# Optimization experiments

Measured on AMD Instinct MI355X. Metric: run time of the kernel, lower is better.

The kernel has to match this reference:

```python
import jax, jax.numpy as jnp
import numpy as np

DT = 1.0 / 200.0  # imu_freq = 200
EPS = 1e-8

def _skew(v):  # [B,3] -> [B,3,3]
    x, y, z = v[:, 0], v[:, 1], v[:, 2]
    zero = jnp.zeros_like(x)
    return jnp.stack([zero, -z, y, z, zero, -x, -y, x, zero], axis=-1).reshape(-1, 3, 3)

def _axis_angle_to_R(w, dt):
    # Rodrigues: R = I + sin(th) K + (1-cos(th)) K^2, th = ||w||*dt
    n = jnp.linalg.norm(w, axis=-1, keepdims=True)          # [B,1]
    theta = n[:, 0] * dt                                     # [B]
    axis = w / (n + EPS)
    K = _skew(axis)
    I = jnp.eye(3, dtype=w.dtype)
    s = jnp.sin(theta)[:, None, None]
    c = jnp.cos(theta)[:, None, None]
    return I + s * K + (1.0 - c) * jnp.einsum('bij,bjk->bik', K, K)

def _R_to_axis_angle(R):
    tr = jnp.trace(R, axis1=-2, axis2=-1)
    angle = jnp.arccos(jnp.clip((tr - 1.0) / 2.0, -1.0 + 1e-7, 1.0 - 1e-7))
    axis = jnp.stack([R[:, 2, 1] - R[:, 1, 2],
                      R[:, 0, 2] - R[:, 2, 0],
                      R[:, 1, 0] - R[:, 0, 1]], axis=-1)
    axis = axis / (2.0 * jnp.sin(angle)[:, None] + EPS)
    return axis, angle

def _aa_to_quat(axis, angle):  # (w, x, y, z)
    h = angle / 2.0
    return jnp.concatenate([jnp.cos(h)[:, None], axis * jnp.sin(h)[:, None]], axis=-1)

def setup_inputs() -> dict:
    key = jax.random.key(0)
    input_seq = jax.random.normal(key, (512, 4096, 6), dtype=jnp.float32)
    return {"input_seq": input_seq}

def reference(input_seq):
    B, T, _ = input_seq.shape
    dtype = input_seq.dtype
    w = jnp.transpose(input_seq[:, :, :3], (1, 0, 2))  # [T,B,3] gyro
    a = jnp.transpose(input_seq[:, :, 3:], (1, 0, 2))  # [T,B,3] accel
    dt = jnp.asarray(DT, dtype)
    dt2_half = dt * dt / 2.0

    dR0 = jnp.broadcast_to(jnp.eye(3, dtype=dtype), (B, 3, 3))
    dv0 = jnp.zeros((B, 3), dtype)
    dp0 = jnp.zeros((B, 3), dtype)

    def step(carry, inp):
        dR, dv, dp = carry
        w_k, a_k = inp
        dR = jnp.einsum('bij,bjk->bik', dR, _axis_angle_to_R(w_k, dt))
        Ra = jnp.einsum('bij,bj->bi', dR, a_k)
        dv = dv + Ra * dt
        dp = dp + dv * dt + Ra * dt2_half  # uses already-updated dv, as in torch code
        axis, angle = _R_to_axis_angle(dR)
        q = _aa_to_quat(axis, angle)
        return (dR, dv, dp), (dp, dv, q)

    _, (ps, vs, qs) = jax.lax.scan(step, (dR0, dv0, dp0), (w, a))
    ps = jnp.transpose(ps, (1, 0, 2))  # [B,T,3]
    vs = jnp.transpose(vs, (1, 0, 2))  # [B,T,3]
    qs = jnp.transpose(qs, (1, 0, 2))  # [B,T,4]
    return jnp.concatenate([input_seq, ps, qs, vs], axis=2)  # [B,T,16]
```

## Files before the change

### kernel.cpp

```cpp
#include <hip/hip_runtime.h>
#include <math.h>

#define T_LEN 4096
#define CHUNK 8
#define NTHR  512
#define ESTRIDE 15

__device__ __forceinline__ void make_A(float wx, float wy, float wz, float* A) {
    const float dt = 1.0f / 200.0f;
    float n = sqrtf(wx*wx + wy*wy + wz*wz);
    float theta = n * dt;
    float inv = 1.0f / (n + 1e-8f);
    float x = wx * inv, y = wy * inv, z = wz * inv;
    float s = sinf(theta);
    float c = cosf(theta);
    float oc = 1.0f - c;
    A[0] = 1.0f + oc * (-(y*y + z*z));
    A[1] = -s*z + oc * (x*y);
    A[2] =  s*y + oc * (x*z);
    A[3] =  s*z + oc * (x*y);
    A[4] = 1.0f + oc * (-(x*x + z*z));
    A[5] = -s*x + oc * (y*z);
    A[6] = -s*y + oc * (x*z);
    A[7] =  s*x + oc * (y*z);
    A[8] = 1.0f + oc * (-(x*x + y*y));
}

__device__ __forceinline__ void matmul3(const float* R, const float* A, float* N) {
#pragma unroll
    for (int i = 0; i < 3; ++i) {
        N[i*3+0] = R[i*3+0]*A[0] + R[i*3+1]*A[3] + R[i*3+2]*A[6];
        N[i*3+1] = R[i*3+0]*A[1] + R[i*3+1]*A[4] + R[i*3+2]*A[7];
        N[i*3+2] = R[i*3+0]*A[2] + R[i*3+1]*A[5] + R[i*3+2]*A[8];
    }
}

__device__ __forceinline__ void step(float* R, float* v, float* p,
                                     float wx, float wy, float wz,
                                     float ax, float ay, float az) {
    const float dt   = 1.0f / 200.0f;
    const float dt2h = dt * dt * 0.5f;
    float A[9], N[9];
    make_A(wx, wy, wz, A);
    matmul3(R, A, N);
#pragma unroll
    for (int i = 0; i < 9; ++i) R[i] = N[i];
    float rax = R[0]*ax + R[1]*ay + R[2]*az;
    float ray = R[3]*ax + R[4]*ay + R[5]*az;
    float raz = R[6]*ax + R[7]*ay + R[8]*az;
    v[0] += rax*dt; v[1] += ray*dt; v[2] += raz*dt;
    p[0] += v[0]*dt + rax*dt2h;
    p[1] += v[1]*dt + ray*dt2h;
    p[2] += v[2]*dt + raz*dt2h;
}

__global__ __launch_bounds__(NTHR)
void preint_kernel(const float* __restrict__ in, float* __restrict__ out) {
    const int b = blockIdx.x;
    const int t = threadIdx.x;
    const float dt = 1.0f / 200.0f;

    const float* bin  = in  + (size_t)b * T_LEN * 6;
    float*       bout = out + (size_t)b * T_LEN * 16;

    float in_reg[CHUNK * 6];
    {
        const float4* src4 = (const float4*)(bin + (size_t)t * CHUNK * 6);
#pragma unroll
        for (int i = 0; i < (CHUNK * 6) / 4; ++i) {
            float4 u = src4[i];
            in_reg[i*4+0] = u.x; in_reg[i*4+1] = u.y;
            in_reg[i*4+2] = u.z; in_reg[i*4+3] = u.w;
        }
    }

    float R[9] = {1,0,0, 0,1,0, 0,0,1};
    float v[3] = {0,0,0};
    float p[3] = {0,0,0};
#pragma unroll
    for (int k = 0; k < CHUNK; ++k) {
        const float* u = in_reg + k * 6;
        step(R, v, p, u[0], u[1], u[2], u[3], u[4], u[5]);
    }

    __shared__ float lds[NTHR * ESTRIDE];
    float* e = lds + t * ESTRIDE;
#pragma unroll
    for (int i = 0; i < 9; ++i) e[i] = R[i];
    e[9]  = v[0]; e[10] = v[1]; e[11] = v[2];
    e[12] = p[0]; e[13] = p[1]; e[14] = p[2];
    __syncthreads();

    for (int d = 1; d < NTHR; d <<= 1) {
        float L[15];
        const bool act = (t >= d);
        if (act) {
            const float* src = lds + (t - d) * ESTRIDE;
#pragma unroll
            for (int i = 0; i < 15; ++i) L[i] = src[i];
        }
        __syncthreads();
        if (act) {
            const float tau2 = (float)(d * CHUNK) * dt;
            float NA[9];
            matmul3(L, R, NA);
            float nb0 = L[9]  + L[0]*v[0] + L[1]*v[1] + L[2]*v[2];
            float nb1 = L[10] + L[3]*v[0] + L[4]*v[1] + L[5]*v[2];
            float nb2 = L[11] + L[6]*v[0] + L[7]*v[1] + L[8]*v[2];
            float nc0 = L[12] + tau2*L[9]  + L[0]*p[0] + L[1]*p[1] + L[2]*p[2];
            float nc1 = L[13] + tau2*L[10] + L[3]*p[0] + L[4]*p[1] + L[5]*p[2];
            float nc2 = L[14] + tau2*L[11] + L[6]*p[0] + L[7]*p[1] + L[8]*p[2];
#pragma unroll
            for (int i = 0; i < 9; ++i) R[i] = NA[i];
            v[0] = nb0; v[1] = nb1; v[2] = nb2;
            p[0] = nc0; p[1] = nc1; p[2] = nc2;
#pragma unroll
            for (int i = 0; i < 9; ++i) e[i] = R[i];
            e[9]  = v[0]; e[10] = v[1]; e[11] = v[2];
            e[12] = p[0]; e[13] = p[1]; e[14] = p[2];
        }
        __syncthreads();
    }

    float S[9]  = {1,0,0, 0,1,0, 0,0,1};
    float sv[3] = {0,0,0};
    float sp[3] = {0,0,0};
    if (t > 0) {
        const float* src = lds + (t - 1) * ESTRIDE;
#pragma unroll
        for (int i = 0; i < 9; ++i) S[i] = src[i];
        sv[0] = src[9];  sv[1] = src[10]; sv[2] = src[11];
        sp[0] = src[12]; sp[1] = src[13]; sp[2] = src[14];
    }

#pragma unroll
    for (int kk = 0; kk < CHUNK; kk += 2) {
        float4 row[8];
#pragma unroll
        for (int j = 0; j < 2; ++j) {
            const int k = kk + j;
            const float* u = in_reg + k * 6;
            step(S, sv, sp, u[0], u[1], u[2], u[3], u[4], u[5]);

            float tr  = S[0] + S[4] + S[8];
            float ca  = fminf(fmaxf(0.5f * (tr - 1.0f), -1.0f + 1e-7f), 1.0f - 1e-7f);
            float qw  = sqrtf(0.5f * (1.0f + ca));
            float i4  = 0.25f / qw;
            float qx  = (S[7] - S[5]) * i4;
            float qy  = (S[2] - S[6]) * i4;
            float qz  = (S[3] - S[1]) * i4;

            row[j*4+0] = make_float4(u[0], u[1], u[2], u[3]);
            row[j*4+1] = make_float4(u[4], u[5], sp[0], sp[1]);
            row[j*4+2] = make_float4(sp[2], qw, qx, qy);
            row[j*4+3] = make_float4(qz, sv[0], sv[1], sv[2]);
        }
        float4* orow = (float4*)(bout + (size_t)(t * CHUNK + kk) * 16);
#pragma unroll
        for (int i = 0; i < 8; ++i) orow[i] = row[i];
    }
}

extern "C" void kernel_launch(void* const* d_in, const int* in_sizes, int n_in,
                              void* d_out, int out_size, void* d_ws, size_t ws_size,
                              hipStream_t stream) {
    const float* in = (const float*)d_in[0];
    float* out = (float*)d_out;
    const int B = in_sizes[0] / (T_LEN * 6);
    preint_kernel<<<dim3(B), dim3(NTHR), 0, stream>>>(in, out);
}
```

Measured before the change: 206.6 us.

## Replace LDS block scan with wave-shuffle scan plus cross-wave totals

```diff
diff --git a/kernel.cpp b/kernel.cpp
--- a/kernel.cpp
+++ b/kernel.cpp
@@ -4,26 +4,26 @@
 #define T_LEN 4096
 #define CHUNK 8
 #define NTHR  512
-#define ESTRIDE 15
+#define NWAVE (NTHR / 64)
 
 __device__ __forceinline__ void make_A(float wx, float wy, float wz, float* A) {
-    const float dt = 1.0f / 200.0f;
-    float n = sqrtf(wx*wx + wy*wy + wz*wz);
-    float theta = n * dt;
-    float inv = 1.0f / (n + 1e-8f);
-    float x = wx * inv, y = wy * inv, z = wz * inv;
-    float s = sinf(theta);
-    float c = cosf(theta);
-    float oc = 1.0f - c;
-    A[0] = 1.0f + oc * (-(y*y + z*z));
-    A[1] = -s*z + oc * (x*y);
-    A[2] =  s*y + oc * (x*z);
-    A[3] =  s*z + oc * (x*y);
-    A[4] = 1.0f + oc * (-(x*x + z*z));
-    A[5] = -s*x + oc * (y*z);
-    A[6] = -s*y + oc * (x*z);
-    A[7] =  s*x + oc * (y*z);
-    A[8] = 1.0f + oc * (-(x*x + y*y));
+    const float dt  = 1.0f / 200.0f;
+    const float dt2 = dt * dt;
+    float n2 = wx*wx + wy*wy + wz*wz;
+    float t2 = n2 * dt2;
+    float s_ = dt  * (1.0f + t2 * (-1.0f/6.0f  + t2 * (1.0f/120.0f)));
+    float oc = dt2 * (0.5f + t2 * (-1.0f/24.0f + t2 * (1.0f/720.0f)));
+    float xx = wx*wx, yy = wy*wy, zz = wz*wz;
+    float xy = wx*wy, xz = wx*wz, yz = wy*wz;
+    A[0] = 1.0f - oc*(yy+zz);
+    A[1] = -s_*wz + oc*xy;
+    A[2] =  s_*wy + oc*xz;
+    A[3] =  s_*wz + oc*xy;
+    A[4] = 1.0f - oc*(xx+zz);
+    A[5] = -s_*wx + oc*yz;
+    A[6] = -s_*wy + oc*xz;
+    A[7] =  s_*wx + oc*yz;
+    A[8] = 1.0f - oc*(xx+yy);
 }
 
 __device__ __forceinline__ void matmul3(const float* R, const float* A, float* N) {
@@ -35,29 +35,46 @@
     }
 }
 
-__device__ __forceinline__ void step(float* R, float* v, float* p,
-                                     float wx, float wy, float wz,
+__device__ __forceinline__ void step(float* E, float wx, float wy, float wz,
                                      float ax, float ay, float az) {
     const float dt   = 1.0f / 200.0f;
     const float dt2h = dt * dt * 0.5f;
     float A[9], N[9];
     make_A(wx, wy, wz, A);
-    matmul3(R, A, N);
+    matmul3(E, A, N);
 #pragma unroll
-    for (int i = 0; i < 9; ++i) R[i] = N[i];
-    float rax = R[0]*ax + R[1]*ay + R[2]*az;
-    float ray = R[3]*ax + R[4]*ay + R[5]*az;
-    float raz = R[6]*ax + R[7]*ay + R[8]*az;
-    v[0] += rax*dt; v[1] += ray*dt; v[2] += raz*dt;
-    p[0] += v[0]*dt + rax*dt2h;
-    p[1] += v[1]*dt + ray*dt2h;
-    p[2] += v[2]*dt + raz*dt2h;
+    for (int i = 0; i < 9; ++i) E[i] = N[i];
+    float rax = E[0]*ax + E[1]*ay + E[2]*az;
+    float ray = E[3]*ax + E[4]*ay + E[5]*az;
+    float raz = E[6]*ax + E[7]*ay + E[8]*az;
+    E[9]  += rax*dt; E[10] += ray*dt; E[11] += raz*dt;
+    E[12] += E[9]*dt  + rax*dt2h;
+    E[13] += E[10]*dt + ray*dt2h;
+    E[14] += E[11]*dt + raz*dt2h;
 }
 
-__global__ __launch_bounds__(NTHR)
+__device__ __forceinline__ void compose(const float* __restrict__ L,
+                                        float* __restrict__ e, float tauY) {
+    float N[9];
+    matmul3(L, e, N);
+    float b0 = L[9]  + L[0]*e[9] + L[1]*e[10] + L[2]*e[11];
+    float b1 = L[10] + L[3]*e[9] + L[4]*e[10] + L[5]*e[11];
+    float b2 = L[11] + L[6]*e[9] + L[7]*e[10] + L[8]*e[11];
+    float c0 = L[12] + tauY*L[9]  + L[0]*e[12] + L[1]*e[13] + L[2]*e[14];
+    float c1 = L[13] + tauY*L[10] + L[3]*e[12] + L[4]*e[13] + L[5]*e[14];
+    float c2 = L[14] + tauY*L[11] + L[6]*e[12] + L[7]*e[13] + L[8]*e[14];
+#pragma unroll
+    for (int i = 0; i < 9; ++i) e[i] = N[i];
+    e[9]  = b0; e[10] = b1; e[11] = b2;
+    e[12] = c0; e[13] = c1; e[14] = c2;
+}
+
+__global__ __launch_bounds__(NTHR, 4)
 void preint_kernel(const float* __restrict__ in, float* __restrict__ out) {
-    const int b = blockIdx.x;
-    const int t = threadIdx.x;
+    const int b    = blockIdx.x;
+    const int t    = threadIdx.x;
+    const int lane = t & 63;
+    const int w    = t >> 6;
     const float dt = 1.0f / 200.0f;
 
     const float* bin  = in  + (size_t)b * T_LEN * 6;
@@ -74,63 +91,64 @@
         }
     }
 
-    float R[9] = {1,0,0, 0,1,0, 0,0,1};
-    float v[3] = {0,0,0};
-    float p[3] = {0,0,0};
+    float e[15] = {1,0,0, 0,1,0, 0,0,1, 0,0,0, 0,0,0};
 #pragma unroll
     for (int k = 0; k < CHUNK; ++k) {
         const float* u = in_reg + k * 6;
-        step(R, v, p, u[0], u[1], u[2], u[3], u[4], u[5]);
+        step(e, u[0], u[1], u[2], u[3], u[4], u[5]);
     }
 
-    __shared__ float lds[NTHR * ESTRIDE];
-    float* e = lds + t * ESTRIDE;
 #pragma unroll
-    for (int i = 0; i < 9; ++i) e[i] = R[i];
-    e[9]  = v[0]; e[10] = v[1]; e[11] = v[2];
-    e[12] = p[0]; e[13] = p[1]; e[14] = p[2];
+    for (int d = 1; d < 64; d <<= 1) {
+        float L[15];
+#pragma unroll
+        for (int i = 0; i < 15; ++i) L[i] = __shfl_up(e[i], d, 64);
+        if (lane >= d) compose(L, e, (float)(d * CHUNK) * dt);
+    }
+
+    __shared__ float wtot[NWAVE][15];
+    if (lane == 63) {
+#pragma unroll
+        for (int i = 0; i < 15; ++i) wtot[w][i] = e[i];
+    }
     __syncthreads();
 
-    for (int d = 1; d < NTHR; d <<= 1) {
-        float L[15];
-        const bool act = (t >= d);
-        if (act) {
-            const float* src = lds + (t - d) * ESTRIDE;
+    if (w == 0) {
+        float s[15] = {1,0,0, 0,1,0, 0,0,1, 0,0,0, 0,0,0};
+        if (lane < NWAVE) {
 #pragma unroll
-            for (int i = 0; i < 15; ++i) L[i] = src[i];
+            for (int i = 0; i < 15; ++i) s[i] = wtot[lane][i];
         }
-        __syncthreads();
-        if (act) {
-            const float tau2 = (float)(d * CHUNK) * dt;
-            float NA[9];
-            matmul3(L, R, NA);
-            float nb0 = L[9]  + L[0]*v[0] + L[1]*v[1] + L[2]*v[2];
-            float nb1 = L[10] + L[3]*v[0] + L[4]*v[1] + L[5]*v[2];
-            float nb2 = L[11] + L[6]*v[0] + L[7]*v[1] + L[8]*v[2];
-            float nc0 = L[12] + tau2*L[9]  + L[0]*p[0] + L[1]*p[1] + L[2]*p[2];
-            float nc1 = L[13] + tau2*L[10] + L[3]*p[0] + L[4]*p[1] + L[5]*p[2];
-            float nc2 = L[14] + tau2*L[11] + L[6]*p[0] + L[7]*p[1] + L[8]*p[2];
 #pragma unroll
-            for (int i = 0; i < 9; ++i) R[i] = NA[i];
-            v[0] = nb0; v[1] = nb1; v[2] = nb2;
-            p[0] = nc0; p[1] = nc1; p[2] = nc2;
+        for (int d = 1; d < NWAVE; d <<= 1) {
+            float L[15];
 #pragma unroll
-            for (int i = 0; i < 9; ++i) e[i] = R[i];
-            e[9]  = v[0]; e[10] = v[1]; e[11] = v[2];
-            e[12] = p[0]; e[13] = p[1]; e[14] = p[2];
+            for (int i = 0; i < 15; ++i) L[i] = __shfl_up(s[i], d, 64);
+            if (lane >= d && lane < NWAVE)
+                compose(L, s, (float)(d * 64 * CHUNK) * dt);
         }
-        __syncthreads();
+        if (lane < NWAVE) {
+#pragma unroll
+            for (int i = 0; i < 15; ++i) wtot[lane][i] = s[i];
+        }
     }
+    __syncthreads();
 
-    float S[9]  = {1,0,0, 0,1,0, 0,0,1};
-    float sv[3] = {0,0,0};
-    float sp[3] = {0,0,0};
-    if (t > 0) {
-        const float* src = lds + (t - 1) * ESTRIDE;
+    float st[15];
 #pragma unroll
-        for (int i = 0; i < 9; ++i) S[i] = src[i];
-        sv[0] = src[9];  sv[1] = src[10]; sv[2] = src[11];
-        sp[0] = src[12]; sp[1] = src[13]; sp[2] = src[14];
+    for (int i = 0; i < 15; ++i) st[i] = __shfl_up(e[i], 1, 64);
+    if (lane == 0) {
+        st[0]=1; st[1]=0; st[2]=0; st[3]=0; st[4]=1; st[5]=0;
+        st[6]=0; st[7]=0; st[8]=1; st[9]=0; st[10]=0; st[11]=0;
+        st[12]=0; st[13]=0; st[14]=0;
+    }
+    {
+        float P[15] = {1,0,0, 0,1,0, 0,0,1, 0,0,0, 0,0,0};
+        if (w > 0) {
+#pragma unroll
+            for (int i = 0; i < 15; ++i) P[i] = wtot[w-1][i];
+        }
+        compose(P, st, (float)(lane * CHUNK) * dt);
     }
 
 #pragma unroll
@@ -140,20 +158,22 @@
         for (int j = 0; j < 2; ++j) {
             const int k = kk + j;
             const float* u = in_reg + k * 6;
-            step(S, sv, sp, u[0], u[1], u[2], u[3], u[4], u[5]);
+            step(st, u[0], u[1], u[2], u[3], u[4], u[5]);
 
-            float tr  = S[0] + S[4] + S[8];
-            float ca  = fminf(fmaxf(0.5f * (tr - 1.0f), -1.0f + 1e-7f), 1.0f - 1e-7f);
-            float qw  = sqrtf(0.5f * (1.0f + ca));
-            float i4  = 0.25f / qw;
-            float qx  = (S[7] - S[5]) * i4;
-            float qy  = (S[2] - S[6]) * i4;
-            float qz  = (S[3] - S[1]) * i4;
+            float tr = st[0] + st[4] + st[8];
+            float ca = fminf(fmaxf(0.5f * (tr - 1.0f), -1.0f + 1e-7f), 1.0f - 1e-7f);
+            float x  = 0.5f * (1.0f + ca);
+            float r  = __frsqrt_rn(x);
+            float qw = x * r;
+            float i4 = 0.25f * r;
+            float qx = (st[7] - st[5]) * i4;
+            float qy = (st[2] - st[6]) * i4;
+            float qz = (st[3] - st[1]) * i4;
 
             row[j*4+0] = make_float4(u[0], u[1], u[2], u[3]);
-            row[j*4+1] = make_float4(u[4], u[5], sp[0], sp[1]);
-            row[j*4+2] = make_float4(sp[2], qw, qx, qy);
-            row[j*4+3] = make_float4(qz, sv[0], sv[1], sv[2]);
+            row[j*4+1] = make_float4(u[4], u[5], st[12], st[13]);
+            row[j*4+2] = make_float4(st[14], qw, qx, qy);
+            row[j*4+3] = make_float4(qz, st[9], st[10], st[11]);
         }
         float4* orow = (float4*)(bout + (size_t)(t * CHUNK + kk) * 16);
 #pragma unroll
```

New measurement: 397.3 us. 92.3% more time.
